# Kernel tuning notes

Hardware: AMD Instinct MI355X
Metric: run time of the kernel (lower is better)

## Reference

```python
import jax, jax.numpy as jnp
import numpy as np

N = 50000      # nodes
E = 800000     # edges (avg degree 16)
F_IN = 128     # num_features
H = 64         # hidden_dim
G = 64         # graphs in batch


def setup_inputs() -> dict:
    key = jax.random.key(0)
    ks = jax.random.split(key, 20)
    inp = {
        "x": jax.random.normal(ks[0], (N, F_IN), jnp.float32),
        "edge_index": jax.random.randint(ks[1], (2, E), 0, N, dtype=jnp.int32).astype(jnp.int64),
        "batch": jnp.sort(jax.random.randint(ks[2], (N,), 0, G, dtype=jnp.int32)).astype(jnp.int64),
    }
    # GraphConv layer dims: in -> out
    dims = [(F_IN, H), (H, 2 * H), (2 * H, 3 * H), (3 * H, H)]
    k = 3
    for i, (din, dout) in enumerate(dims):
        s = 1.0 / np.sqrt(din).astype(np.float32)
        inp[f"w{i+1}_rel"] = jax.random.normal(ks[k], (din, dout), jnp.float32) * s
        inp[f"w{i+1}_root"] = jax.random.normal(ks[k + 1], (din, dout), jnp.float32) * s
        inp[f"b{i+1}"] = jnp.zeros((dout,), jnp.float32)
        k += 2
    inp["head_w"] = jax.random.normal(ks[k], (H, 1), jnp.float32) * (1.0 / np.sqrt(H).astype(np.float32))
    inp["head_b"] = jnp.zeros((1,), jnp.float32)
    return inp


def _graph_conv(x, src, dst, w_rel, w_root, b):
    # PyG GraphConv: out = lin_rel(sum_{j in N(i)} x_j) + lin_root(x_i)
    agg = jax.ops.segment_sum(x[src], dst, num_segments=N)  # [N, din]
    return agg @ w_rel + b + x @ w_root


def reference(x, edge_index, batch,
              w1_rel, w1_root, b1,
              w2_rel, w2_root, b2,
              w3_rel, w3_root, b3,
              w4_rel, w4_root, b4,
              head_w, head_b):
    src, dst = edge_index[0], edge_index[1]
    h = jax.nn.relu(_graph_conv(x, src, dst, w1_rel, w1_root, b1))
    h = jax.nn.relu(_graph_conv(h, src, dst, w2_rel, w2_root, b2))
    h = jax.nn.relu(_graph_conv(h, src, dst, w3_rel, w3_root, b3))
    h = _graph_conv(h, src, dst, w4_rel, w4_root, b4)          # [N, H]
    # global_mean_pool over graph ids
    sums = jax.ops.segment_sum(h, batch, num_segments=G)       # [G, H]
    counts = jax.ops.segment_sum(jnp.ones((N,), h.dtype), batch, num_segments=G)
    pooled = sums / jnp.maximum(counts, 1.0)[:, None]          # [G, H]
    return pooled @ head_w + head_b                            # [G, 1]
```

## Files before the change

kernel.cpp:

```cpp
#include <hip/hip_runtime.h>


#define NNODES 50000
#define NEDGES 800000
#define NGRAPH 64
#define NBUK 256
#define BSZ 196
#define EPB (NEDGES / NBUK)
#define CVT_NB (NNODES * 128 / 4 / 256)
#define PACK_NB (160 * 512 / 256)

typedef __attribute__((ext_vector_type(8))) __bf16 bf16x8;
typedef __attribute__((ext_vector_type(16))) float f32x16;

__device__ __forceinline__ unsigned short f2bf(float f) {
    unsigned u = __float_as_uint(f);
    u += 0x7fff + ((u >> 16) & 1);
    return (unsigned short)(u >> 16);
}
__device__ __forceinline__ float bf2f(unsigned b) {
    return __uint_as_float(b << 16);
}


__global__ void hist_kernel(const int* __restrict__ dst, int* __restrict__ cnt) {
    __shared__ int h[NBUK];
    int tid = threadIdx.x, k = blockIdx.x;
    h[tid] = 0;
    __syncthreads();
    int end = (k + 1) * EPB;
    for (int i = k * EPB + tid; i < end; i += 256)
        atomicAdd(&h[dst[i] / BSZ], 1);
    __syncthreads();
    cnt[tid * NBUK + k] = h[tid];
}

__global__ void scan1_kernel(int* __restrict__ a, int* __restrict__ bsum, int n) {
    __shared__ int buf[256];
    int tid = threadIdx.x;
    int i = blockIdx.x * 256 + tid;
    int v = (i < n) ? a[i] : 0;
    buf[tid] = v;
    __syncthreads();
    #pragma unroll
    for (int off = 1; off < 256; off <<= 1) {
        int t = (tid >= off) ? buf[tid - off] : 0;
        __syncthreads();
        buf[tid] += t;
        __syncthreads();
    }
    if (i < n) a[i] = buf[tid] - v;
    if (tid == 255) bsum[blockIdx.x] = buf[255];
}

__global__ void scan2_kernel(int* __restrict__ bsum, int nb) {
    __shared__ int buf[256];
    int tid = threadIdx.x;
    int v = (tid < nb) ? bsum[tid] : 0;
    buf[tid] = v;
    __syncthreads();
    #pragma unroll
    for (int off = 1; off < 256; off <<= 1) {
        int t = (tid >= off) ? buf[tid - off] : 0;
        __syncthreads();
        buf[tid] += t;
        __syncthreads();
    }
    if (tid < nb) bsum[tid] = buf[tid] - v;
}

__global__ void scan3_kernel(int* __restrict__ a, const int* __restrict__ bsum, int n) {
    int i = blockIdx.x * 256 + threadIdx.x;
    if (i < n) a[i] += bsum[blockIdx.x];
}

__global__ void partition_kernel(const int* __restrict__ src, const int* __restrict__ dst,
                                 const int* __restrict__ cnt,
                                 unsigned long long* __restrict__ pedge) {
    __shared__ int lbase[NBUK];
    int tid = threadIdx.x, k = blockIdx.x;
    lbase[tid] = cnt[tid * NBUK + k];
    __syncthreads();
    int end = (k + 1) * EPB;
    for (int i = k * EPB + tid; i < end; i += 256) {
        int s = src[i], d = dst[i];
        int pos = atomicAdd(&lbase[d / BSZ], 1);
        pedge[pos] = (unsigned long long)(unsigned)s | ((unsigned long long)(unsigned)d << 32);
    }
}

__global__ void build_kernel(const unsigned long long* __restrict__ pedge,
                             const int* __restrict__ cnt,
                             int* __restrict__ rp, int* __restrict__ csr) {
    __shared__ int sdeg[256], sc[256], sbase[256], sfill[256];
    int tid = threadIdx.x, b = blockIdx.x;
    int node0 = b * BSZ;
    int ncnt = NNODES - node0;
    if (ncnt > BSZ) ncnt = BSZ;
    if (ncnt < 0) ncnt = 0;
    int seg0 = cnt[b * NBUK];
    int seg1 = (b + 1 < NBUK) ? cnt[(b + 1) * NBUK] : NEDGES;
    sdeg[tid] = 0;
    sfill[tid] = 0;
    __syncthreads();
    for (int i = seg0 + tid; i < seg1; i += 256)
        atomicAdd(&sdeg[(int)(pedge[i] >> 32) - node0], 1);
    __syncthreads();
    sc[tid] = sdeg[tid];
    __syncthreads();
    #pragma unroll
    for (int off = 1; off < 256; off <<= 1) {
        int t = (tid >= off) ? sc[tid - off] : 0;
        __syncthreads();
        sc[tid] += t;
        __syncthreads();
    }
    sbase[tid] = sc[tid] - sdeg[tid];
    if (tid < ncnt) rp[node0 + tid] = seg0 + sbase[tid];
    if (b == NBUK - 1 && tid == 0) rp[NNODES] = NEDGES;
    __syncthreads();
    for (int i = seg0 + tid; i < seg1; i += 256) {
        unsigned long long p = pedge[i];
        int d = (int)(p >> 32) - node0;
        int pos = atomicAdd(&sfill[d], 1);
        csr[seg0 + sbase[d] + pos] = (int)(p & 0xffffffffu);
    }
}


__device__ __forceinline__ void pack32(const float* __restrict__ W, unsigned short* __restrict__ dst,
                                       int KS_tot, int ks0, int dcols, int ct0,
                                       int tl, int ksl, int lane, int j) {
    int k = ksl * 16 + ((lane >> 5) << 3) + j;
    int col = tl * 32 + (lane & 31);
    dst[(((size_t)(ct0 + tl) * KS_tot + (ks0 + ksl)) * 64 + lane) * 8 + j] = f2bf(W[k * dcols + col]);
}

__global__ void prep_kernel(const float* __restrict__ x, unsigned short* __restrict__ xbf,
                            const float* __restrict__ w1_rel, const float* __restrict__ w1_root,
                            const float* __restrict__ w2_rel, const float* __restrict__ w2_root,
                            const float* __restrict__ w3_rel, const float* __restrict__ w3_root,
                            unsigned short* __restrict__ pL1, unsigned short* __restrict__ pL2,
                            unsigned short* __restrict__ pL3,
                            const float* __restrict__ w4_rel, const float* __restrict__ w4_root,
                            const float* __restrict__ b4, const float* __restrict__ head_w,
                            float* __restrict__ wr, float* __restrict__ wt,
                            float* __restrict__ cbuf) {
    int b = blockIdx.x;
    int tid = threadIdx.x;
    if (b < CVT_NB) {
        int i = b * 256 + tid;
        float4 v = ((const float4*)x)[i];
        unsigned lo = (unsigned)f2bf(v.x) | ((unsigned)f2bf(v.y) << 16);
        unsigned hi = (unsigned)f2bf(v.z) | ((unsigned)f2bf(v.w) << 16);
        ((uint2*)xbf)[i] = make_uint2(lo, hi);
    } else if (b < CVT_NB + PACK_NB) {
        int idx = (b - CVT_NB) * 256 + tid;
        int g = idx >> 9;
        int t = idx & 511;
        int lane = (t >> 3) & 63, j = t & 7;
        if (g < 16)       { int gl = g;       pack32(w1_rel,  pL1, 8,  0, 64,  0, gl / 8, gl % 8, lane, j); }
        else if (g < 32)  { int gl = g - 16;  pack32(w1_root, pL1, 8,  0, 64,  2, gl / 8, gl % 8, lane, j); }
        else if (g < 48)  { int gl = g - 32;  pack32(w2_rel,  pL2, 8,  0, 128, 0, gl / 4, gl % 4, lane, j); }
        else if (g < 64)  { int gl = g - 48;  pack32(w2_root, pL2, 8,  4, 128, 0, gl / 4, gl % 4, lane, j); }
        else if (g < 112) { int gl = g - 64;  pack32(w3_rel,  pL3, 16, 0, 192, 0, gl / 8, gl % 8, lane, j); }
        else              { int gl = g - 112; pack32(w3_root, pL3, 16, 8, 192, 0, gl / 8, gl % 8, lane, j); }
    } else {
        if (tid < 192) {
            float ar = 0.f, at = 0.f;
            for (int j = 0; j < 64; j++) {
                float hw = head_w[j];
                ar = fmaf(w4_rel[tid * 64 + j], hw, ar);
                at = fmaf(w4_root[tid * 64 + j], hw, at);
            }
            wr[tid] = ar;
            wt[tid] = at;
        } else if (tid == 192) {
            float c = 0.f;
            for (int j = 0; j < 64; j++) c = fmaf(b4[j], head_w[j], c);
            cbuf[0] = c;
        }
    }
}


template<int NT, int KS>
__global__ __launch_bounds__(256) void gemm32_kernel(
    const unsigned short* __restrict__ A, const unsigned short* __restrict__ W,
    const float* __restrict__ bias, unsigned short* __restrict__ OUT,
    int ldo, int ocol0, int relu, int N)
{
    const int K = KS * 16;
    int tid = threadIdx.x;
    int wave = tid >> 6, lane = tid & 63;
    int l32 = lane & 31, half = lane >> 5;
    int rbase = blockIdx.x * 128 + wave * 32;
    if (rbase >= N) return;

    int arow = rbase + l32;
    if (arow >= N) arow = N - 1;
    const unsigned short* ab = A + (size_t)arow * K + half * 8;

    f32x16 acc[NT];
    #pragma unroll
    for (int t = 0; t < NT; t++)
        #pragma unroll
        for (int r = 0; r < 16; r++) acc[t][r] = 0.f;

    bf16x8 a_cur = *(const bf16x8*)(ab);
    #pragma unroll
    for (int ks = 0; ks < KS; ks++) {
        bf16x8 a_nxt;
        if (ks + 1 < KS) a_nxt = *(const bf16x8*)(ab + (ks + 1) * 16);
        #pragma unroll
        for (int t = 0; t < NT; t++) {
            bf16x8 b = *(const bf16x8*)(W + ((size_t)(t * KS + ks) * 64 + lane) * 8);
            acc[t] = __builtin_amdgcn_mfma_f32_32x32x16_bf16(a_cur, b, acc[t], 0, 0, 0);
        }
        a_cur = a_nxt;
    }

    #pragma unroll
    for (int t = 0; t < NT; t++) {
        int col = t * 32 + l32;
        float bi = bias ? bias[col] : 0.f;
        #pragma unroll
        for (int reg = 0; reg < 16; reg++) {
            int row = rbase + (reg & 3) + 8 * (reg >> 2) + 4 * half;
            if (row < N) {
                float v = acc[t][reg] + bi;
                if (relu) v = fmaxf(v, 0.f);
                OUT[(size_t)row * ldo + ocol0 + col] = f2bf(v);
            }
        }
    }
}


__device__ __forceinline__ void acc8(float* a, uint4 u) {
    a[0] += bf2f(u.x & 0xffffu); a[1] += bf2f(u.x >> 16);
    a[2] += bf2f(u.y & 0xffffu); a[3] += bf2f(u.y >> 16);
    a[4] += bf2f(u.z & 0xffffu); a[5] += bf2f(u.z >> 16);
    a[6] += bf2f(u.w & 0xffffu); a[7] += bf2f(u.w >> 16);
}

template<int LPF>
__global__ void agg_kernel_v2(const unsigned short* __restrict__ X, int ldx,
                              const int* __restrict__ rp, const int* __restrict__ csr,
                              const unsigned short* __restrict__ root, int ldr,
                              const float* __restrict__ bias, int relu,
                              unsigned short* __restrict__ OUT, int ldo, int N) {
    int t = blockIdx.x * blockDim.x + threadIdx.x;
    int node = t / (2 * LPF);
    int r = t % (2 * LPF);
    int sub = r / LPF;
    int sl = r % LPF;
    if (node >= N) return;
    float a[8] = {0.f, 0.f, 0.f, 0.f, 0.f, 0.f, 0.f, 0.f};
    int e0 = rp[node], e1 = rp[node + 1];
    const unsigned short* xb = X + 8 * sl;
    int e = e0 + sub;
    for (; e + 2 < e1; e += 4) {
        int s0 = csr[e], s1 = csr[e + 2];
        uint4 u0 = *(const uint4*)(xb + (size_t)s0 * ldx);
        uint4 u1 = *(const uint4*)(xb + (size_t)s1 * ldx);
        acc8(a, u0);
        acc8(a, u1);
    }
    if (e < e1) {
        uint4 u = *(const uint4*)(xb + (size_t)csr[e] * ldx);
        acc8(a, u);
    }
    #pragma unroll
    for (int i = 0; i < 8; i++) a[i] += __shfl_xor(a[i], LPF, 64);
    if (sub == 0) {
        if (root) {
            uint4 u = *(const uint4*)(root + (size_t)node * ldr + 8 * sl);
            acc8(a, u);
        }
        if (bias) {
            float4 b0 = *(const float4*)(bias + 8 * sl);
            float4 b1 = *(const float4*)(bias + 8 * sl + 4);
            a[0] += b0.x; a[1] += b0.y; a[2] += b0.z; a[3] += b0.w;
            a[4] += b1.x; a[5] += b1.y; a[6] += b1.z; a[7] += b1.w;
        }
        if (relu) {
            #pragma unroll
            for (int i = 0; i < 8; i++) a[i] = fmaxf(a[i], 0.f);
        }
        uint4 o;
        o.x = (unsigned)f2bf(a[0]) | ((unsigned)f2bf(a[1]) << 16);
        o.y = (unsigned)f2bf(a[2]) | ((unsigned)f2bf(a[3]) << 16);
        o.z = (unsigned)f2bf(a[4]) | ((unsigned)f2bf(a[5]) << 16);
        o.w = (unsigned)f2bf(a[6]) | ((unsigned)f2bf(a[7]) << 16);
        *(uint4*)(OUT + (size_t)node * ldo + 8 * sl) = o;
    }
}


__global__ void st_kernel(const unsigned short* __restrict__ h3, const float* __restrict__ wr,
                          const float* __restrict__ wt, float* __restrict__ s,
                          float* __restrict__ t, int N) {
    int lane = threadIdx.x & 63;
    int node = (blockIdx.x * blockDim.x + threadIdx.x) >> 6;
    if (node >= N) return;
    float as = 0.f, at = 0.f;
    if (lane < 48) {
        uint2 u = *(const uint2*)(h3 + (size_t)node * 192 + 4 * lane);
        float x0 = bf2f(u.x & 0xffffu), x1 = bf2f(u.x >> 16);
        float x2 = bf2f(u.y & 0xffffu), x3 = bf2f(u.y >> 16);
        float4 r4 = *(const float4*)(wr + 4 * lane);
        float4 t4 = *(const float4*)(wt + 4 * lane);
        as = x0 * r4.x + x1 * r4.y + x2 * r4.z + x3 * r4.w;
        at = x0 * t4.x + x1 * t4.y + x2 * t4.z + x3 * t4.w;
    }
    #pragma unroll
    for (int off = 32; off > 0; off >>= 1) {
        as += __shfl_down(as, off, 64);
        at += __shfl_down(at, off, 64);
    }
    if (lane == 0) { s[node] = as; t[node] = at; }
}

__global__ void aggpool_kernel(const float* __restrict__ s, const float* __restrict__ t,
                               const int* __restrict__ rp, const int* __restrict__ csr,
                               const int* __restrict__ batch, float* __restrict__ gsum,
                               int* __restrict__ cnt, int N) {
    __shared__ float ls[NGRAPH];
    __shared__ int lc[NGRAPH];
    int tid = threadIdx.x;
    if (tid < NGRAPH) { ls[tid] = 0.f; lc[tid] = 0; }
    __syncthreads();
    int n = blockIdx.x * blockDim.x + tid;
    if (n < N) {
        float a = 0.f;
        int e = rp[n], e1 = rp[n + 1];
        for (; e + 3 < e1; e += 4) {
            int s0 = csr[e], s1 = csr[e + 1], s2 = csr[e + 2], s3 = csr[e + 3];
            a += s[s0] + s[s1] + s[s2] + s[s3];
        }
        for (; e < e1; e++) a += s[csr[e]];
        int g = batch[n];
        atomicAdd(&ls[g], a + t[n]);
        atomicAdd(&lc[g], 1);
    }
    __syncthreads();
    if (tid < NGRAPH && lc[tid] > 0) {
        atomicAdd(&gsum[tid], ls[tid]);
        atomicAdd(&cnt[tid], lc[tid]);
    }
}

__global__ void final_kernel(const float* __restrict__ gsum, const int* __restrict__ cnt,
                             const float* __restrict__ cbuf, const float* __restrict__ head_b,
                             float* __restrict__ out) {
    int g = threadIdx.x;
    if (g < NGRAPH) {
        float c = (float)(cnt[g] > 0 ? cnt[g] : 1);
        out[g] = gsum[g] / c + cbuf[0] + head_b[0];
    }
}


extern "C" void kernel_launch(void* const* d_in, const int* in_sizes, int n_in,
                              void* d_out, int out_size, void* d_ws, size_t ws_size,
                              hipStream_t stream) {
    const float* x       = (const float*)d_in[0];
    const int*   edge    = (const int*)d_in[1];
    const int*   batch   = (const int*)d_in[2];
    const float* w1_rel  = (const float*)d_in[3];
    const float* w1_root = (const float*)d_in[4];
    const float* b1      = (const float*)d_in[5];
    const float* w2_rel  = (const float*)d_in[6];
    const float* w2_root = (const float*)d_in[7];
    const float* b2      = (const float*)d_in[8];
    const float* w3_rel  = (const float*)d_in[9];
    const float* w3_root = (const float*)d_in[10];
    const float* b3      = (const float*)d_in[11];
    const float* w4_rel  = (const float*)d_in[12];
    const float* w4_root = (const float*)d_in[13];
    const float* b4      = (const float*)d_in[14];
    const float* head_w  = (const float*)d_in[15];
    const float* head_b  = (const float*)d_in[16];
    float* out = (float*)d_out;

    const int N = NNODES, E = NEDGES;
    const int* src = edge;
    const int* dst = edge + E;

    char* ws = (char*)d_ws;
    size_t off = 0;
    auto alloc = [&](size_t bytes) -> char* {
        char* p = ws + off;
        off = (off + bytes + 255) & ~(size_t)255;
        return p;
    };
    float* gsum  = (float*)alloc(NGRAPH * 4);
    int*   cnt   = (int*)alloc(NGRAPH * 4);
    size_t zero_bytes = off;
    int*   bcnt  = (int*)alloc((size_t)NBUK * NBUK * 4);
    int*   bsum  = (int*)alloc(256 * 4);
    int*   rp    = (int*)alloc((size_t)(N + 1) * 4);
    int*   csr   = (int*)alloc((size_t)E * 4);
    unsigned long long* pedge = (unsigned long long*)alloc((size_t)E * 8);
    unsigned short* xbf    = (unsigned short*)alloc((size_t)N * 128 * 2);
    unsigned short* z1     = (unsigned short*)alloc((size_t)N * 128 * 2);
    unsigned short* combo2 = (unsigned short*)alloc((size_t)N * 128 * 2);
    unsigned short* combo3 = (unsigned short*)alloc((size_t)N * 256 * 2);
    unsigned short* h3     = (unsigned short*)alloc((size_t)N * 192 * 2);
    unsigned short* pL1    = (unsigned short*)alloc(4 * 8 * 512 * 2);
    unsigned short* pL2    = (unsigned short*)alloc(4 * 8 * 512 * 2);
    unsigned short* pL3    = (unsigned short*)alloc(6 * 16 * 512 * 2);
    float* sbuf  = (float*)alloc((size_t)N * 4);
    float* tbuf  = (float*)alloc((size_t)N * 4);
    float* wr    = (float*)alloc(192 * 4);
    float* wt    = (float*)alloc(192 * 4);
    float* cbuf  = (float*)alloc(4);
    (void)ws_size;

    hipMemsetAsync(gsum, 0, zero_bytes, stream);

    const int TB = 256;

    hist_kernel<<<NBUK, 256, 0, stream>>>(dst, bcnt);
    scan1_kernel<<<NBUK, 256, 0, stream>>>(bcnt, bsum, NBUK * NBUK);
    scan2_kernel<<<1, 256, 0, stream>>>(bsum, NBUK);
    scan3_kernel<<<NBUK, 256, 0, stream>>>(bcnt, bsum, NBUK * NBUK);
    partition_kernel<<<NBUK, 256, 0, stream>>>(src, dst, bcnt, pedge);
    build_kernel<<<NBUK, 256, 0, stream>>>(pedge, bcnt, rp, csr);

    prep_kernel<<<CVT_NB + PACK_NB + 1, 256, 0, stream>>>(
        x, xbf, w1_rel, w1_root, w2_rel, w2_root, w3_rel, w3_root,
        pL1, pL2, pL3, w4_rel, w4_root, b4, head_w, wr, wt, cbuf);

    int ggrid = (N + 127) / 128;

    gemm32_kernel<4, 8><<<ggrid, 256, 0, stream>>>(xbf, pL1, nullptr, z1, 128, 0, 0, N);
    agg_kernel_v2<8><<<(N * 16 + TB - 1) / TB, TB, 0, stream>>>(z1, 128, rp, csr,
                                                                z1 + 64, 128, b1, 1, combo2 + 64, 128, N);
    agg_kernel_v2<8><<<(N * 16 + TB - 1) / TB, TB, 0, stream>>>(combo2 + 64, 128, rp, csr,
                                                                nullptr, 0, nullptr, 0, combo2, 128, N);
    gemm32_kernel<4, 8><<<ggrid, 256, 0, stream>>>(combo2, pL2, b2, combo3, 256, 128, 1, N);
    agg_kernel_v2<16><<<(N * 32 + TB - 1) / TB, TB, 0, stream>>>(combo3 + 128, 256, rp, csr,
                                                                 nullptr, 0, nullptr, 0, combo3, 256, N);
    gemm32_kernel<6, 16><<<ggrid, 256, 0, stream>>>(combo3, pL3, b3, h3, 192, 0, 1, N);

    st_kernel<<<(N * 64 + TB - 1) / TB, TB, 0, stream>>>(h3, wr, wt, sbuf, tbuf, N);
    aggpool_kernel<<<(N + TB - 1) / TB, TB, 0, stream>>>(sbuf, tbuf, rp, csr, batch, gsum, cnt, N);
    final_kernel<<<1, 64, 0, stream>>>(gsum, cnt, cbuf, head_b, out);
}
```

Before: 293.7 us.

## Stage GEMM weights in LDS, compute two row tiles per wave, split wide layer

The GEMM kernel now copies its packed weight tile into shared memory once per block and has each wave compute two 32-row MFMA tiles that share every B fragment. Blocks shrink to 128 threads. The 192-column third layer is split into two 96-column halves across twice as many blocks to limit register pressure. This aims to cut redundant global weight loads and raise MFMA work per load, at the cost of a per-block LDS fill, a block barrier, and more accumulator registers.

```diff
diff --git a/kernel.cpp b/kernel.cpp
--- a/kernel.cpp
+++ b/kernel.cpp
@@ -184,53 +184,84 @@
 }
 
 
-template<int NT, int KS>
-__global__ __launch_bounds__(256) void gemm32_kernel(
-    const unsigned short* __restrict__ A, const unsigned short* __restrict__ W,
+template<int NT, int KS, int NHALF>
+__global__ __launch_bounds__(128, 2) void gemm_v3(
+    const unsigned short* __restrict__ A, const unsigned short* __restrict__ Wall,
     const float* __restrict__ bias, unsigned short* __restrict__ OUT,
-    int ldo, int ocol0, int relu, int N)
+    int ldo, int ocol_base, int relu, int N)
 {
     const int K = KS * 16;
+    __shared__ unsigned short sB[NT * KS * 512];
+
+    int b = blockIdx.x;
+    int halfsel = 0;
+    if (NHALF == 2) {
+        int nblk = gridDim.x >> 1;
+        halfsel = (b >= nblk) ? 1 : 0;
+        b -= halfsel * nblk;
+    }
+    const unsigned short* W = Wall + (size_t)halfsel * NT * KS * 512;
+
     int tid = threadIdx.x;
     int wave = tid >> 6, lane = tid & 63;
     int l32 = lane & 31, half = lane >> 5;
-    int rbase = blockIdx.x * 128 + wave * 32;
-    if (rbase >= N) return;
-
-    int arow = rbase + l32;
-    if (arow >= N) arow = N - 1;
-    const unsigned short* ab = A + (size_t)arow * K + half * 8;
-
-    f32x16 acc[NT];
-    #pragma unroll
-    for (int t = 0; t < NT; t++)
+
+    {
+        const uint4* gsrc = (const uint4*)W;
+        uint4* ldst = (uint4*)sB;
+        const int total = NT * KS * 64;
+        #pragma unroll 4
+        for (int i = tid; i < total; i += 128) ldst[i] = gsrc[i];
+    }
+
+    int rbase = b * 128 + wave * 64;
+    int ar0 = rbase + l32;        if (ar0 >= N) ar0 = N - 1;
+    int ar1 = rbase + 32 + l32;   if (ar1 >= N) ar1 = N - 1;
+    const unsigned short* a0p = A + (size_t)ar0 * K + half * 8;
+    const unsigned short* a1p = A + (size_t)ar1 * K + half * 8;
+
+    __syncthreads();
+
+    f32x16 acc[2][NT];
+    #pragma unroll
+    for (int m = 0; m < 2; m++)
         #pragma unroll
-        for (int r = 0; r < 16; r++) acc[t][r] = 0.f;
-
-    bf16x8 a_cur = *(const bf16x8*)(ab);
+        for (int t = 0; t < NT; t++)
+            #pragma unroll
+            for (int r = 0; r < 16; r++) acc[m][t][r] = 0.f;
+
+    bf16x8 a0 = *(const bf16x8*)a0p;
+    bf16x8 a1 = *(const bf16x8*)a1p;
     #pragma unroll
     for (int ks = 0; ks < KS; ks++) {
-        bf16x8 a_nxt;
-        if (ks + 1 < KS) a_nxt = *(const bf16x8*)(ab + (ks + 1) * 16);
+        bf16x8 a0n = a0, a1n = a1;
+        if (ks + 1 < KS) {
+            a0n = *(const bf16x8*)(a0p + (ks + 1) * 16);
+            a1n = *(const bf16x8*)(a1p + (ks + 1) * 16);
+        }
         #pragma unroll
         for (int t = 0; t < NT; t++) {
-            bf16x8 b = *(const bf16x8*)(W + ((size_t)(t * KS + ks) * 64 + lane) * 8);
-            acc[t] = __builtin_amdgcn_mfma_f32_32x32x16_bf16(a_cur, b, acc[t], 0, 0, 0);
-        }
-        a_cur = a_nxt;
-    }
-
-    #pragma unroll
-    for (int t = 0; t < NT; t++) {
-        int col = t * 32 + l32;
-        float bi = bias ? bias[col] : 0.f;
+            bf16x8 bb = *(const bf16x8*)(sB + (size_t)(t * KS + ks) * 512 + lane * 8);
+            acc[0][t] = __builtin_amdgcn_mfma_f32_32x32x16_bf16(a0, bb, acc[0][t], 0, 0, 0);
+            acc[1][t] = __builtin_amdgcn_mfma_f32_32x32x16_bf16(a1, bb, acc[1][t], 0, 0, 0);
+        }
+        a0 = a0n; a1 = a1n;
+    }
+
+    #pragma unroll
+    for (int m = 0; m < 2; m++) {
         #pragma unroll
-        for (int reg = 0; reg < 16; reg++) {
-            int row = rbase + (reg & 3) + 8 * (reg >> 2) + 4 * half;
-            if (row < N) {
-                float v = acc[t][reg] + bi;
-                if (relu) v = fmaxf(v, 0.f);
-                OUT[(size_t)row * ldo + ocol0 + col] = f2bf(v);
+        for (int t = 0; t < NT; t++) {
+            int laycol = halfsel * NT * 32 + t * 32 + l32;
+            float bi = bias ? bias[laycol] : 0.f;
+            #pragma unroll
+            for (int reg = 0; reg < 16; reg++) {
+                int row = rbase + m * 32 + (reg & 3) + 8 * (reg >> 2) + 4 * half;
+                if (row < N) {
+                    float v = acc[m][t][reg] + bi;
+                    if (relu) v = fmaxf(v, 0.f);
+                    OUT[(size_t)row * ldo + ocol_base + laycol] = f2bf(v);
+                }
             }
         }
     }
@@ -435,15 +466,15 @@
 
     int ggrid = (N + 127) / 128;
 
-    gemm32_kernel<4, 8><<<ggrid, 256, 0, stream>>>(xbf, pL1, nullptr, z1, 128, 0, 0, N);
+    gemm_v3<4, 8, 1><<<ggrid, 128, 0, stream>>>(xbf, pL1, nullptr, z1, 128, 0, 0, N);
     agg_kernel_v2<8><<<(N * 16 + TB - 1) / TB, TB, 0, stream>>>(z1, 128, rp, csr,
                                                                 z1 + 64, 128, b1, 1, combo2 + 64, 128, N);
     agg_kernel_v2<8><<<(N * 16 + TB - 1) / TB, TB, 0, stream>>>(combo2 + 64, 128, rp, csr,
                                                                 nullptr, 0, nullptr, 0, combo2, 128, N);
-    gemm32_kernel<4, 8><<<ggrid, 256, 0, stream>>>(combo2, pL2, b2, combo3, 256, 128, 1, N);
+    gemm_v3<4, 8, 1><<<ggrid, 128, 0, stream>>>(combo2, pL2, b2, combo3, 256, 128, 1, N);
     agg_kernel_v2<16><<<(N * 32 + TB - 1) / TB, TB, 0, stream>>>(combo3 + 128, 256, rp, csr,
                                                                  nullptr, 0, nullptr, 0, combo3, 256, N);
-    gemm32_kernel<6, 16><<<ggrid, 256, 0, stream>>>(combo3, pL3, b3, h3, 192, 0, 1, N);
+    gemm_v3<3, 16, 2><<<2 * ggrid, 128, 0, stream>>>(combo3, pL3, b3, h3, 192, 0, 1, N);
 
     st_kernel<<<(N * 64 + TB - 1) / TB, TB, 0, stream>>>(h3, wr, wt, sbuf, tbuf, N);
     aggpool_kernel<<<(N + TB - 1) / TB, TB, 0, stream>>>(sbuf, tbuf, rp, csr, batch, gsum, cnt, N);
```

Result: slower. 305.0 us (+3.8%).
